# Optimization experiments

Measured on AMD Instinct MI355X. Metric: run time of the kernel, lower is better.

Reference implementation:

```python
import jax, jax.numpy as jnp
import numpy as np

G = 8192          # graphs per hand side (PyG batch)
J_SRC = 17        # source-hand joints (transform: Linear(17*64, 13*64))
J_TGT = 13        # target-hand joints
NEG_SLOPE = 0.01  # F.leaky_relu default


def _chain_edge_index(J, num_graphs):
    # bidirectional chain tree per graph, block-diagonal batched like PyG
    p = np.arange(J - 1); c = np.arange(1, J)
    src = np.concatenate([p, c]); dst = np.concatenate([c, p])
    base = np.arange(num_graphs)[:, None] * J
    return jnp.asarray(np.stack([(src[None] + base).ravel(), (dst[None] + base).ravel()]), jnp.int32)


def _lin_init(key, o, i):
    k1, k2 = jax.random.split(key)
    s = 1.0 / np.sqrt(i)
    return (jax.random.uniform(k1, (o, i), jnp.float32, -s, s),
            jax.random.uniform(k2, (o,), jnp.float32, -s, s))


def setup_inputs() -> dict:
    key = jax.random.key(0)
    ks = iter(jax.random.split(key, 64))
    inp = {}
    Nl = G * J_SRC
    inp["l_hand_x"] = jax.random.normal(next(ks), (Nl, 3), jnp.float32)
    inp["r_hand_x"] = jax.random.normal(next(ks), (Nl, 3), jnp.float32)
    ei_src = _chain_edge_index(J_SRC, G)
    inp["l_hand_edge_index"] = ei_src
    inp["r_hand_edge_index"] = ei_src
    E_src = ei_src.shape[1]
    inp["l_hand_edge_attr"] = jax.random.normal(next(ks), (E_src, 3), jnp.float32)
    inp["r_hand_edge_attr"] = jax.random.normal(next(ks), (E_src, 3), jnp.float32)
    ei_t = _chain_edge_index(J_TGT, G)
    inp["hand_edge_index"] = ei_t
    inp["hand_edge_attr"] = jax.random.normal(next(ks), (ei_t.shape[1], 6), jnp.float32)
    Nt = G * J_TGT
    inp["hand_lower"] = -(jax.random.uniform(next(ks), (Nt, 1), jnp.float32) + 0.5)
    inp["hand_upper"] = jax.random.uniform(next(ks), (Nt, 1), jnp.float32) + 0.5
    inp["hand_offset"] = jax.random.normal(next(ks), (Nt, 3), jnp.float32) * 0.05
    ax = jax.random.normal(next(ks), (Nt, 3), jnp.float32)
    inp["hand_axis"] = ax / jnp.linalg.norm(ax, axis=-1, keepdims=True)
    par = np.concatenate([[-1], np.arange(J_TGT - 1)])  # chain: root then parents
    inp["hand_parent"] = jnp.asarray(np.tile(par, G), jnp.int32)
    inp["num_graphs"] = G
    dims = {"enc1_lin": (16, 9),  "enc1_up": (16, 3),
            "enc2_lin": (32, 35), "enc2_up": (32, 16),
            "enc3_lin": (64, 67), "enc3_up": (64, 32),
            "trans":    (13 * 64, 17 * 64),
            "dec1_lin": (32, 138), "dec1_up": (32, 66),
            "dec2_lin": (16, 70),  "dec2_up": (16, 32),
            "dec3_lin": (1, 38),   "dec3_up": (1, 16)}
    for n, (o, i) in dims.items():
        W, b = _lin_init(next(ks), o, i)
        inp[n + "_W"] = W; inp[n + "_b"] = b
    return inp


def _block(x, ei, ea, Wl, bl, Wu, bu):
    # SpatialBasicBlock: gather x_i/x_j, concat edge_attr, linear+leaky_relu,
    # scatter-add at target nodes, residual upsample of x.
    src, dst = ei[0], ei[1]
    z = jnp.concatenate([x[dst], x[src], ea], axis=-1)  # [E, 2*in+edge]
    m = jax.nn.leaky_relu(z @ Wl.T + bl, NEG_SLOPE)
    agg = jax.ops.segment_sum(m, dst, num_segments=x.shape[0])
    return agg + x @ Wu.T + bu


def _rodrigues(ax, ang):
    # rotation matrices about unit axis ax [...,3] by angle ang [...]
    c = jnp.cos(ang)[..., None, None]; s = jnp.sin(ang)[..., None, None]
    I = jnp.eye(3, dtype=ax.dtype)
    aa = ax[..., :, None] * ax[..., None, :]
    x, y, z = ax[..., 0], ax[..., 1], ax[..., 2]
    zero = jnp.zeros_like(x)
    K = jnp.stack([jnp.stack([zero, -z, y], -1),
                   jnp.stack([z, zero, -x], -1),
                   jnp.stack([-y, x, zero], -1)], -2)
    return c * I + (1 - c) * aa + s * K


def _fk(ang, parent, offset, axis, num_graphs, J):
    # forward kinematics along parent chain (parent[j] < j, root = -1)
    a = ang.reshape(num_graphs, J)
    off = offset.reshape(num_graphs, J, 3)
    ax = axis.reshape(num_graphs, J, 3)
    par = parent.reshape(num_graphs, J)[0]  # same topology in every graph
    Rl = _rodrigues(ax, a)                  # [G, J, 3, 3] local rotations
    I = jnp.eye(3, dtype=ang.dtype)
    pos = jnp.zeros((num_graphs, J, 3), ang.dtype)
    rot = jnp.zeros((num_graphs, J, 3, 3), ang.dtype)
    for j in range(J):  # J=13 fixed structural loop
        p = par[j]
        root = p < 0
        Rp = jnp.where(root, I, jnp.take(rot, p, axis=1))
        Pp = jnp.where(root, 0.0, jnp.take(pos, p, axis=1))
        pos = pos.at[:, j].set(Pp + jnp.einsum('gab,gb->ga', Rp, off[:, j]))
        rot = rot.at[:, j].set(jnp.einsum('gab,gbc->gac', Rp, Rl[:, j]))
    return pos.reshape(-1, 3)


def reference(l_hand_x, r_hand_x, l_hand_edge_index, r_hand_edge_index,
              l_hand_edge_attr, r_hand_edge_attr, hand_edge_index, hand_edge_attr,
              hand_lower, hand_upper, hand_offset, hand_axis, hand_parent, num_graphs,
              enc1_lin_W, enc1_lin_b, enc1_up_W, enc1_up_b,
              enc2_lin_W, enc2_lin_b, enc2_up_W, enc2_up_b,
              enc3_lin_W, enc3_lin_b, enc3_up_W, enc3_up_b,
              trans_W, trans_b,
              dec1_lin_W, dec1_lin_b, dec1_up_W, dec1_up_b,
              dec2_lin_W, dec2_lin_b, dec2_up_W, dec2_up_b,
              dec3_lin_W, dec3_lin_b, dec3_up_W, dec3_up_b):
    # ---- encode ----
    Nl = l_hand_x.shape[0]
    x = jnp.concatenate([l_hand_x, r_hand_x], axis=0)
    ei = jnp.concatenate([l_hand_edge_index, r_hand_edge_index + Nl], axis=1)
    ea = jnp.concatenate([l_hand_edge_attr, r_hand_edge_attr], axis=0)
    h = _block(x, ei, ea, enc1_lin_W, enc1_lin_b, enc1_up_W, enc1_up_b)
    h = _block(h, ei, ea, enc2_lin_W, enc2_lin_b, enc2_up_W, enc2_up_b)
    h = _block(h, ei, ea, enc3_lin_W, enc3_lin_b, enc3_up_W, enc3_up_b)
    G2 = 2 * num_graphs
    z = jnp.tanh(h.reshape(G2, -1) @ trans_W.T + trans_b).reshape(-1, 64)
    # ---- decode ----
    half = z.shape[0] // 2
    ei_t = jnp.concatenate([hand_edge_index, hand_edge_index + half], axis=1)
    ea_t = jnp.concatenate([hand_edge_attr, hand_edge_attr], axis=0)
    lower = jnp.concatenate([hand_lower, hand_lower], axis=0)
    upper = jnp.concatenate([hand_upper, hand_upper], axis=0)
    offset = jnp.concatenate([hand_offset, hand_offset], axis=0)
    axis = jnp.concatenate([hand_axis, hand_axis], axis=0)
    parent = jnp.concatenate([hand_parent, hand_parent], axis=0)
    xd = jnp.concatenate([z, lower, upper], axis=1)  # [2*G*13, 66]
    h = _block(xd, ei_t, ea_t, dec1_lin_W, dec1_lin_b, dec1_up_W, dec1_up_b)
    h = _block(h, ei_t, ea_t, dec2_lin_W, dec2_lin_b, dec2_up_W, dec2_up_b)
    ang = jnp.tanh(_block(h, ei_t, ea_t, dec3_lin_W, dec3_lin_b, dec3_up_W, dec3_up_b))
    ang = lower + (upper - lower) * (ang + 1) / 2
    pos = _fk(ang, parent, offset, axis, G2, J_TGT)
    hn = ang.shape[0] // 2
    return ang[:hn], pos[:hn], ang[hn:], pos[hn:]
```

## Files before the change

kernel.cpp:

```cpp
#include <hip/hip_runtime.h>
#include <math.h>


constexpr int G_NUM = 8192;
constexpr int JS = 17;
constexpr int JT = 13;
constexpr int N_ENC = 2 * G_NUM * JS;
constexpr int N_DEC = 2 * G_NUM * JT;
constexpr int G2 = 2 * G_NUM;
constexpr int HN = G_NUM * JT;
constexpr int K_TR = JS * 64;
constexpr int N_TR = JT * 64;

typedef unsigned short u16;
typedef u16   u16x8 __attribute__((ext_vector_type(8)));
typedef u16   u16x4 __attribute__((ext_vector_type(4)));
typedef float f32x4 __attribute__((ext_vector_type(4)));
typedef __bf16 bf16x8 __attribute__((ext_vector_type(8)));

__device__ __forceinline__ float lrelu(float v) { return v > 0.f ? v : 0.01f * v; }
__device__ __forceinline__ u16 f2bf(float f) {
    unsigned u = __float_as_uint(f);
    u += 0x7fff + ((u >> 16) & 1);
    return (u16)(u >> 16);
}
__device__ __forceinline__ float bf2f(u16 h) { return __uint_as_float((unsigned)h << 16); }

template<int K_MM, int C_IN_W, int C_OUT, int C_E, int J, int G, bool TAIL>
__global__ __launch_bounds__(256)
void block_mfma(const u16* __restrict__ xHi, const u16* __restrict__ xLo,
                const float* __restrict__ eaA, const float* __restrict__ eaB, int g_half,
                const float* __restrict__ lowv, const float* __restrict__ upv,
                const float* __restrict__ Wl, const float* __restrict__ bl,
                const float* __restrict__ Wu, const float* __restrict__ bu,
                u16* __restrict__ outHi, u16* __restrict__ outLo)
{
    constexpr int ROWS = G * J;
    constexpr int F = (ROWS + 15) / 16;
    constexpr int NCH = C_OUT / 16;
    constexpr int KF = K_MM / 32;
    constexpr int KPAD = K_MM + 8;
    constexpr int EAS = 2 * (J - 1) * C_E;
    constexpr int CTOT = 2 * C_IN_W + C_E;
    constexpr int CW = (C_IN_W < K_MM) ? C_IN_W : K_MM;
    constexpr int WGG = 4 * G;

    __shared__ __align__(16) u16 sWH[3 * C_OUT * KPAD], sWL[3 * C_OUT * KPAD];
    __shared__ float sEA[WGG * EAS];
    __shared__ float sWe[C_OUT * C_E];
    __shared__ float sBl[C_OUT], sBu[C_OUT];
    __shared__ float sTl[TAIL ? 6 * C_OUT : 1];
    __shared__ float sLow[TAIL ? WGG * J : 1], sUpp[TAIL ? WGG * J : 1];

    const int t = threadIdx.x;
    const int g0 = blockIdx.x * WGG;

    for (int i = t; i < 3 * C_OUT * K_MM; i += 256) {
        const int ch = i / K_MM, k = i % K_MM;
        const int p = ch / C_OUT, o = ch % C_OUT;
        float v = 0.f;
        if (k < CW) {
            if (p == 0)      v = Wl[o * CTOT + k];
            else if (p == 1) v = Wl[o * CTOT + C_IN_W + k];
            else             v = Wu[o * C_IN_W + k];
        }
        const u16 h = f2bf(v);
        sWH[ch * KPAD + k] = h;
        sWL[ch * KPAD + k] = f2bf(v - bf2f(h));
    }
    for (int i = t; i < WGG * EAS; i += 256) {
        const int lg = i / EAS, r = i % EAS;
        const int g = g0 + lg;
        sEA[i] = (g < g_half) ? eaA[(size_t)g * EAS + r]
                              : eaB[(size_t)(g - g_half) * EAS + r];
    }
    for (int i = t; i < C_OUT * C_E; i += 256)
        sWe[i] = Wl[(i / C_E) * CTOT + 2 * C_IN_W + (i % C_E)];
    if (t < C_OUT) { sBl[t] = bl[t]; sBu[t] = bu[t]; }
    if constexpr (TAIL) {
        if (t < C_OUT) {
            sTl[t * 6 + 0] = Wl[t * CTOT + K_MM];
            sTl[t * 6 + 1] = Wl[t * CTOT + K_MM + 1];
            sTl[t * 6 + 2] = Wl[t * CTOT + C_IN_W + K_MM];
            sTl[t * 6 + 3] = Wl[t * CTOT + C_IN_W + K_MM + 1];
            sTl[t * 6 + 4] = Wu[t * C_IN_W + K_MM];
            sTl[t * 6 + 5] = Wu[t * C_IN_W + K_MM + 1];
        }
        for (int i = t; i < WGG * J; i += 256) {
            const int lg = i / J, j = i % J;
            const int g = g0 + lg;
            const int ge = (g < g_half) ? g : g - g_half;
            sLow[i] = lowv[ge * J + j];
            sUpp[i] = upv[ge * J + j];
        }
    }
    __syncthreads();

    const int wv = t >> 6, lane = t & 63;
    const int col = lane & 15, kg = lane >> 4;
    const size_t baseNode = (size_t)(blockIdx.x * 4 + wv) * ROWS;
    const int lgB = wv * G;

    for (int ch = 0; ch < NCH; ++ch) {
        const int o = ch * 16 + col;
        bf16x8 wUh[KF], wUl[KF], wVh[KF], wVl[KF], wPh[KF], wPl[KF];
        #pragma unroll
        for (int kf = 0; kf < KF; ++kf) {
            wUh[kf] = *(const bf16x8*)&sWH[(0 * C_OUT + o) * KPAD + kf * 32 + kg * 8];
            wUl[kf] = *(const bf16x8*)&sWL[(0 * C_OUT + o) * KPAD + kf * 32 + kg * 8];
            wVh[kf] = *(const bf16x8*)&sWH[(1 * C_OUT + o) * KPAD + kf * 32 + kg * 8];
            wVl[kf] = *(const bf16x8*)&sWL[(1 * C_OUT + o) * KPAD + kf * 32 + kg * 8];
            wPh[kf] = *(const bf16x8*)&sWH[(2 * C_OUT + o) * KPAD + kf * 32 + kg * 8];
            wPl[kf] = *(const bf16x8*)&sWL[(2 * C_OUT + o) * KPAD + kf * 32 + kg * 8];
        }
        float we[C_E];
        #pragma unroll
        for (int k = 0; k < C_E; ++k) we[k] = sWe[o * C_E + k];
        const float blo = sBl[o], buo = sBu[o];
        float tl0 = 0, tl1 = 0, tl2 = 0, tl3 = 0, tl4 = 0, tl5 = 0;
        if constexpr (TAIL) {
            tl0 = sTl[o * 6 + 0]; tl1 = sTl[o * 6 + 1]; tl2 = sTl[o * 6 + 2];
            tl3 = sTl[o * 6 + 3]; tl4 = sTl[o * 6 + 4]; tl5 = sTl[o * 6 + 5];
        }

        f32x4 Vpp = {0,0,0,0}, Vp = {0,0,0,0};
        f32x4 Up = {0,0,0,0}, Pp = {0,0,0,0};
        #pragma unroll
        for (int f = 0; f <= F; ++f) {
            f32x4 Vc = {0,0,0,0}, Uc = {0,0,0,0}, Pc = {0,0,0,0};
            if (f < F) {
                const int nrow = f * 16 + col;
                const size_t nd = baseNode + (nrow < ROWS ? nrow : ROWS - 1);
                #pragma unroll
                for (int kf = 0; kf < KF; ++kf) {
                    const bf16x8 aH = *(const bf16x8*)&xHi[nd * K_MM + kf * 32 + kg * 8];
                    const bf16x8 aL = *(const bf16x8*)&xLo[nd * K_MM + kf * 32 + kg * 8];
                    Vc = __builtin_amdgcn_mfma_f32_16x16x32_bf16(aH, wVh[kf], Vc, 0, 0, 0);
                    Vc = __builtin_amdgcn_mfma_f32_16x16x32_bf16(aH, wVl[kf], Vc, 0, 0, 0);
                    Vc = __builtin_amdgcn_mfma_f32_16x16x32_bf16(aL, wVh[kf], Vc, 0, 0, 0);
                    Uc = __builtin_amdgcn_mfma_f32_16x16x32_bf16(aH, wUh[kf], Uc, 0, 0, 0);
                    Uc = __builtin_amdgcn_mfma_f32_16x16x32_bf16(aH, wUl[kf], Uc, 0, 0, 0);
                    Uc = __builtin_amdgcn_mfma_f32_16x16x32_bf16(aL, wUh[kf], Uc, 0, 0, 0);
                    Pc = __builtin_amdgcn_mfma_f32_16x16x32_bf16(aH, wPh[kf], Pc, 0, 0, 0);
                    Pc = __builtin_amdgcn_mfma_f32_16x16x32_bf16(aH, wPl[kf], Pc, 0, 0, 0);
                    Pc = __builtin_amdgcn_mfma_f32_16x16x32_bf16(aL, wPh[kf], Pc, 0, 0, 0);
                }
            }
            if (f >= 1) {
                const int fm = f - 1;
                const float vL0a = __shfl(Vpp[3], 48 + col);
                const float vL0b = __shfl(Vp[3], (lane - 16) & 63);
                const float vL0 = (kg == 0) ? vL0a : vL0b;
                const float vR3a = __shfl(Vc[0], col);
                const float vR3b = __shfl(Vp[0], (lane + 16) & 63);
                const float vR3 = (kg == 3) ? vR3a : vR3b;
                #pragma unroll
                for (int r = 0; r < 4; ++r) {
                    const int row = fm * 16 + kg * 4 + r;
                    const bool valid = row < ROWS;
                    const int jpos = row % J;
                    int gl = row / J; if (gl > G - 1) gl = G - 1;
                    const int lg = lgB + gl;
                    const bool h1m = valid && (jpos > 0);
                    const bool h2m = valid && (jpos < J - 1);
                    const int jm = jpos > 0 ? jpos - 1 : 0;
                    float e1 = 0.f, e2 = 0.f;
                    #pragma unroll
                    for (int k = 0; k < C_E; ++k) {
                        e1 = fmaf(we[k], sEA[lg * EAS + jm * C_E + k], e1);
                        e2 = fmaf(we[k], sEA[lg * EAS + (J - 1 + jpos) * C_E + k], e2);
                    }
                    float vL = (r == 0) ? vL0 : Vp[r - 1];
                    float vR = (r == 3) ? vR3 : Vp[r + 1];
                    float u = Up[r], p = Pp[r];
                    if constexpr (TAIL) {
                        const int jp = jpos < J - 1 ? jpos + 1 : J - 1;
                        u = fmaf(tl0, sLow[lg * J + jpos], u);
                        u = fmaf(tl1, sUpp[lg * J + jpos], u);
                        p = fmaf(tl4, sLow[lg * J + jpos], p);
                        p = fmaf(tl5, sUpp[lg * J + jpos], p);
                        vL = fmaf(tl2, sLow[lg * J + jm], vL);
                        vL = fmaf(tl3, sUpp[lg * J + jm], vL);
                        vR = fmaf(tl2, sLow[lg * J + jp], vR);
                        vR = fmaf(tl3, sUpp[lg * J + jp], vR);
                    }
                    const float m1 = u + vL + e1 + blo;
                    const float m2 = u + vR + e2 + blo;
                    const float res = p + buo + (h1m ? lrelu(m1) : 0.f) + (h2m ? lrelu(m2) : 0.f);
                    if (valid) {
                        const size_t node = baseNode + row;
                        const u16 hh = f2bf(res);
                        outHi[node * C_OUT + o] = hh;
                        outLo[node * C_OUT + o] = f2bf(res - bf2f(hh));
                    }
                }
            }
            Vpp = Vp; Vp = Vc; Up = Uc; Pp = Pc;
        }
    }
}

template<int C_IN, int C_OUT, int C_E, int J, int NN, int OPAD>
__global__ __launch_bounds__(256)
void block_small(const float* __restrict__ xA, const float* __restrict__ xB, int node_half,
                 const float* __restrict__ eaA, const float* __restrict__ eaB, int g_half,
                 const float* __restrict__ Wl, const float* __restrict__ bl,
                 const float* __restrict__ Wu, const float* __restrict__ bu,
                 u16* __restrict__ outHi, u16* __restrict__ outLo, int N)
{
    constexpr int CTOT = 2 * C_IN + C_E;
    constexpr int SOP = C_OUT + 1;
    constexpr int NPB = 256 / C_OUT;
    __shared__ float wl_T[CTOT * SOP];
    __shared__ float wu_T[C_IN * SOP];
    __shared__ float bl_s[C_OUT], bu_s[C_OUT];
    const int t = threadIdx.x;
    for (int i = t; i < C_OUT * CTOT; i += 256) { int oo = i / CTOT, kk = i % CTOT; wl_T[kk * SOP + oo] = Wl[i]; }
    for (int i = t; i < C_OUT * C_IN; i += 256) { int oo = i / C_IN, kk = i % C_IN; wu_T[kk * SOP + oo] = Wu[i]; }
    if (t < C_OUT) { bl_s[t] = bl[t]; bu_s[t] = bu[t]; }
    __syncthreads();

    const int o = t % C_OUT;
    const int s = t / C_OUT;
    const int nb = (blockIdx.x * NPB + s) * NN;
    float up[NN], m1[NN], m2[NN];
    #pragma unroll
    for (int i = 0; i < NN; ++i) { up[i] = bu_s[o]; m1[i] = bl_s[o]; m2[i] = bl_s[o]; }
    auto clampn = [&](int nd) { return nd < 0 ? 0 : (nd >= N ? N - 1 : nd); };

    for (int k = 0; k < C_IN; ++k) {
        const float w0 = wl_T[k * SOP + o];
        const float w1 = wl_T[(C_IN + k) * SOP + o];
        const float wuv = wu_T[k * SOP + o];
        float xs[NN + 2];
        #pragma unroll
        for (int i = 0; i < NN + 2; ++i) {
            const int nd = clampn(nb - 1 + i);
            xs[i] = (nd < node_half) ? xA[(size_t)nd * C_IN + k]
                                     : xB[(size_t)(nd - node_half) * C_IN + k];
        }
        #pragma unroll
        for (int nd = 0; nd < NN; ++nd) {
            up[nd] = fmaf(wuv, xs[nd + 1], up[nd]);
            m1[nd] = fmaf(w0, xs[nd + 1], m1[nd]);
            m1[nd] = fmaf(w1, xs[nd], m1[nd]);
            m2[nd] = fmaf(w0, xs[nd + 1], m2[nd]);
            m2[nd] = fmaf(w1, xs[nd + 2], m2[nd]);
        }
    }
    #pragma unroll
    for (int nd = 0; nd < NN; ++nd) {
        const int node = nb + nd;
        const int g = node / J;
        const int j = node - g * J;
        const bool has1 = (j > 0), has2 = (j < J - 1);
        const int geff = (g < g_half) ? g : g - g_half;
        const float* ea = (g < g_half) ? eaA : eaB;
        const ptrdiff_t e1 = ((ptrdiff_t)geff * 2 * (J - 1) + (j - 1)) * C_E;
        const ptrdiff_t e2 = ((ptrdiff_t)geff * 2 * (J - 1) + (J - 1) + j) * C_E;
        float a1 = m1[nd], a2 = m2[nd];
        #pragma unroll
        for (int k = 0; k < C_E; ++k) {
            const float w = wl_T[(2 * C_IN + k) * SOP + o];
            if (has1) a1 = fmaf(w, ea[e1 + k], a1);
            if (has2) a2 = fmaf(w, ea[e2 + k], a2);
        }
        const float v = up[nd] + (has1 ? lrelu(a1) : 0.f) + (has2 ? lrelu(a2) : 0.f);
        const u16 hh = f2bf(v);
        outHi[(size_t)node * OPAD + o] = hh;
        outLo[(size_t)node * OPAD + o] = f2bf(v - bf2f(hh));
        if (OPAD > C_OUT) {
            outHi[(size_t)node * OPAD + o + C_OUT] = 0;
            outLo[(size_t)node * OPAD + o + C_OUT] = 0;
        }
    }
}

__device__ __forceinline__ void trans_step(const u16* __restrict__ sWHb,
                                           const u16* __restrict__ sWLb,
                                           const u16x8* __restrict__ a,
                                           int wn, int lr, int kg, f32x4 acc[4][2])
{
    bf16x8 bh[2], bl2[2];
    #pragma unroll
    for (int n = 0; n < 2; ++n) {
        const int r = wn * 32 + n * 16 + lr;
        bh[n]  = *(const bf16x8*)&sWHb[r * 40 + kg * 8];
        bl2[n] = *(const bf16x8*)&sWLb[r * 40 + kg * 8];
    }
    #pragma unroll
    for (int m = 0; m < 4; ++m) {
        const bf16x8 ah = __builtin_bit_cast(bf16x8, a[2 * m]);
        const bf16x8 al = __builtin_bit_cast(bf16x8, a[2 * m + 1]);
        #pragma unroll
        for (int n = 0; n < 2; ++n) {
            acc[m][n] = __builtin_amdgcn_mfma_f32_16x16x32_bf16(ah, bh[n],  acc[m][n], 0, 0, 0);
            acc[m][n] = __builtin_amdgcn_mfma_f32_16x16x32_bf16(ah, bl2[n], acc[m][n], 0, 0, 0);
            acc[m][n] = __builtin_amdgcn_mfma_f32_16x16x32_bf16(al, bh[n],  acc[m][n], 0, 0, 0);
        }
    }
}

__global__ __launch_bounds__(256)
void trans_mfma(const u16* __restrict__ aHi, const u16* __restrict__ aLo,
                const float* __restrict__ W, const float* __restrict__ bias,
                u16* __restrict__ zHi, u16* __restrict__ zLo)
{
    constexpr int NI = K_TR / 32;
    __shared__ __align__(16) u16 sWH[2][64 * 40], sWL[2][64 * 40];
    const int t = threadIdx.x, lane = t & 63, w = t >> 6;
    const int wm = w >> 1, wn = w & 1, lr = lane & 15, kg = lane >> 4;
    const int bm = blockIdx.x * 128, bn = blockIdx.y * 64;
    const int swr = t >> 2, swc = (t & 3) * 8;

    auto stageW = [&](int i, int buf) {
        const int k0 = i * 32;
        const float4 f0 = *(const float4*)&W[(size_t)(bn + swr) * K_TR + k0 + swc];
        const float4 f1 = *(const float4*)&W[(size_t)(bn + swr) * K_TR + k0 + swc + 4];
        const float fv[8] = {f0.x, f0.y, f0.z, f0.w, f1.x, f1.y, f1.z, f1.w};
        u16x8 hq, lq;
        #pragma unroll
        for (int j = 0; j < 8; ++j) {
            const u16 h = f2bf(fv[j]);
            hq[j] = h;
            lq[j] = f2bf(fv[j] - bf2f(h));
        }
        *(u16x8*)&sWH[buf][swr * 40 + swc] = hq;
        *(u16x8*)&sWL[buf][swr * 40 + swc] = lq;
    };
    u16x8 aA[8], aB[8];
    auto gloadA = [&](int i, u16x8* dst) {
        const int k0 = i * 32;
        #pragma unroll
        for (int m = 0; m < 4; ++m) {
            const size_t off = (size_t)(bm + wm * 64 + m * 16 + lr) * K_TR + k0 + kg * 8;
            dst[2 * m]     = *(const u16x8*)&aHi[off];
            dst[2 * m + 1] = *(const u16x8*)&aLo[off];
        }
    };

    f32x4 acc[4][2];
    #pragma unroll
    for (int m = 0; m < 4; ++m)
        #pragma unroll
        for (int n = 0; n < 2; ++n) acc[m][n] = f32x4{0.f, 0.f, 0.f, 0.f};

    stageW(0, 0);
    gloadA(0, aA);
    __syncthreads();
    for (int i = 0; i < NI; i += 2) {
        if (i + 1 < NI) { stageW(i + 1, 1); gloadA(i + 1, aB); }
        trans_step(sWH[0], sWL[0], aA, wn, lr, kg, acc);
        __syncthreads();
        if (i + 2 < NI) { stageW(i + 2, 0); gloadA(i + 2, aA); }
        trans_step(sWH[1], sWL[1], aB, wn, lr, kg, acc);
        __syncthreads();
    }

    #pragma unroll
    for (int n = 0; n < 2; ++n) {
        const int colz = bn + wn * 32 + n * 16 + lr;
        const float bv = bias[colz];
        #pragma unroll
        for (int m = 0; m < 4; ++m)
            #pragma unroll
            for (int r = 0; r < 4; ++r) {
                const int row = bm + wm * 64 + m * 16 + kg * 4 + r;
                const float v = tanhf(acc[m][n][r] + bv);
                const size_t idx = (size_t)row * N_TR + colz;
                const u16 hh = f2bf(v);
                zHi[idx] = hh;
                zLo[idx] = f2bf(v - bf2f(hh));
            }
    }
}

__global__ __launch_bounds__(256)
void dec3fk_kernel(const u16* __restrict__ xHi, const u16* __restrict__ xLo,
                   const float* __restrict__ ea,
                   const float* __restrict__ Wl, const float* __restrict__ bl,
                   const float* __restrict__ Wu, const float* __restrict__ bu,
                   const float* __restrict__ lowv, const float* __restrict__ upv,
                   const float* __restrict__ offset, const float* __restrict__ axis,
                   float* __restrict__ dout)
{
    const int g2 = blockIdx.x * 256 + threadIdx.x;
    if (g2 >= G2) return;
    const int geff = (g2 >= G_NUM) ? g2 - G_NUM : g2;
    const bool rightH = (g2 >= G_NUM);

    auto loadrow = [&](int nd, float* x) {
        const u16x8 h0 = *(const u16x8*)&xHi[(size_t)nd * 16];
        const u16x8 h1 = *(const u16x8*)&xHi[(size_t)nd * 16 + 8];
        const u16x8 l0 = *(const u16x8*)&xLo[(size_t)nd * 16];
        const u16x8 l1 = *(const u16x8*)&xLo[(size_t)nd * 16 + 8];
        #pragma unroll
        for (int k = 0; k < 8; ++k) {
            x[k]     = bf2f(h0[k]) + bf2f(l0[k]);
            x[k + 8] = bf2f(h1[k]) + bf2f(l1[k]);
        }
    };

    float xprev[16], xcur[16], xnext[16];
    #pragma unroll
    for (int k = 0; k < 16; ++k) xprev[k] = 0.f;
    loadrow(g2 * JT, xcur);
    loadrow(g2 * JT + 1, xnext);

    float R[9];
    float px = 0.f, py = 0.f, pz = 0.f;
    for (int j = 0; j < JT; ++j) {
        const int node = g2 * JT + j;
        const bool has1 = (j > 0), has2 = (j < JT - 1);
        float m1 = bl[0], m2 = m1, up = bu[0];
        #pragma unroll
        for (int k = 0; k < 16; ++k) {
            const float xd = xcur[k];
            up = fmaf(Wu[k], xd, up);
            const float w0 = Wl[k];
            m1 = fmaf(w0, xd, m1);
            m2 = fmaf(w0, xd, m2);
            const float w1 = Wl[16 + k];
            m1 = fmaf(w1, xprev[k], m1);
            m2 = fmaf(w1, xnext[k], m2);
        }
        const int e1 = (geff * 24 + (j - 1)) * 6;
        const int e2 = (geff * 24 + 12 + j) * 6;
        #pragma unroll
        for (int k = 0; k < 6; ++k) {
            const float ww = Wl[32 + k];
            if (has1) m1 = fmaf(ww, ea[e1 + k], m1);
            if (has2) m2 = fmaf(ww, ea[e2 + k], m2);
        }
        const float v = up + (has1 ? lrelu(m1) : 0.f) + (has2 ? lrelu(m2) : 0.f);
        const int idx = geff * JT + j;
        const float lo = lowv[idx], hi = upv[idx];
        const float a = lo + (hi - lo) * (tanhf(v) + 1.f) * 0.5f;
        if (!rightH) dout[node] = a;
        else         dout[4 * HN + idx] = a;

        const float ax = axis[idx * 3], ay = axis[idx * 3 + 1], az = axis[idx * 3 + 2];
        const float ox = offset[idx * 3], oy = offset[idx * 3 + 1], oz = offset[idx * 3 + 2];
        const float c = cosf(a), s = sinf(a), ic = 1.f - c;
        const float L[9] = {
            c + ic * ax * ax,      ic * ax * ay - s * az, ic * ax * az + s * ay,
            ic * ay * ax + s * az, c + ic * ay * ay,      ic * ay * az - s * ax,
            ic * az * ax - s * ay, ic * az * ay + s * ax, c + ic * az * az };
        if (j == 0) {
            px = ox; py = oy; pz = oz;
            #pragma unroll
            for (int q = 0; q < 9; ++q) R[q] = L[q];
        } else {
            px += R[0] * ox + R[1] * oy + R[2] * oz;
            py += R[3] * ox + R[4] * oy + R[5] * oz;
            pz += R[6] * ox + R[7] * oy + R[8] * oz;
            float T[9];
            #pragma unroll
            for (int r = 0; r < 3; ++r)
                #pragma unroll
                for (int cc = 0; cc < 3; ++cc)
                    T[r * 3 + cc] = R[r * 3] * L[cc] + R[r * 3 + 1] * L[3 + cc] + R[r * 3 + 2] * L[6 + cc];
            #pragma unroll
            for (int q = 0; q < 9; ++q) R[q] = T[q];
        }
        const int pbase = (!rightH) ? (HN + node * 3) : (5 * HN + idx * 3);
        dout[pbase] = px; dout[pbase + 1] = py; dout[pbase + 2] = pz;

        #pragma unroll
        for (int k = 0; k < 16; ++k) { xprev[k] = xcur[k]; xcur[k] = xnext[k]; }
        const int nn = node + 2 < N_DEC ? node + 2 : N_DEC - 1;
        if (j < JT - 1) loadrow(nn, xnext);
    }
}

extern "C" void kernel_launch(void* const* d_in, const int* in_sizes, int n_in,
                              void* d_out, int out_size, void* d_ws, size_t ws_size,
                              hipStream_t stream)
{
    const float* l_x  = (const float*)d_in[0];
    const float* r_x  = (const float*)d_in[1];
    const float* l_ea = (const float*)d_in[4];
    const float* r_ea = (const float*)d_in[5];
    const float* ea_t = (const float*)d_in[7];
    const float* lowv = (const float*)d_in[8];
    const float* upv  = (const float*)d_in[9];
    const float* offs = (const float*)d_in[10];
    const float* axis = (const float*)d_in[11];
    const float* e1lW = (const float*)d_in[14]; const float* e1lB = (const float*)d_in[15];
    const float* e1uW = (const float*)d_in[16]; const float* e1uB = (const float*)d_in[17];
    const float* e2lW = (const float*)d_in[18]; const float* e2lB = (const float*)d_in[19];
    const float* e2uW = (const float*)d_in[20]; const float* e2uB = (const float*)d_in[21];
    const float* e3lW = (const float*)d_in[22]; const float* e3lB = (const float*)d_in[23];
    const float* e3uW = (const float*)d_in[24]; const float* e3uB = (const float*)d_in[25];
    const float* trW  = (const float*)d_in[26]; const float* trB  = (const float*)d_in[27];
    const float* d1lW = (const float*)d_in[28]; const float* d1lB = (const float*)d_in[29];
    const float* d1uW = (const float*)d_in[30]; const float* d1uB = (const float*)d_in[31];
    const float* d2lW = (const float*)d_in[32]; const float* d2lB = (const float*)d_in[33];
    const float* d2uW = (const float*)d_in[34]; const float* d2uB = (const float*)d_in[35];
    const float* d3lW = (const float*)d_in[36]; const float* d3lB = (const float*)d_in[37];
    const float* d3uW = (const float*)d_in[38]; const float* d3uB = (const float*)d_in[39];

    char* ws = (char*)d_ws;
    u16* h1H  = (u16*)(ws + 0);          u16* h1L  = (u16*)(ws + 17825792);
    u16* h2H  = (u16*)(ws + 71303168);   u16* h2L  = (u16*)(ws + 89128960);
    u16* aH   = (u16*)(ws + 0);          u16* aL   = (u16*)(ws + 35651584);
    u16* zzH  = (u16*)(ws + 71303168);   u16* zzL  = (u16*)(ws + 98566144);
    u16* hd1H = (u16*)(ws + 0);          u16* hd1L = (u16*)(ws + 13631488);
    u16* hd2H = (u16*)(ws + 27262976);   u16* hd2L = (u16*)(ws + 34078720);
    float* outp = (float*)d_out;

    block_small<3, 16, 3, JS, 4, 32><<<N_ENC / 64, 256, 0, stream>>>(
        l_x, r_x, G_NUM * JS, l_ea, r_ea, G_NUM,
        e1lW, e1lB, e1uW, e1uB, h1H, h1L, N_ENC);
    block_mfma<32, 16, 32, 3, JS, 4, false><<<1024, 256, 0, stream>>>(
        h1H, h1L, l_ea, r_ea, G_NUM, nullptr, nullptr,
        e2lW, e2lB, e2uW, e2uB, h2H, h2L);
    block_mfma<32, 32, 64, 3, JS, 4, false><<<1024, 256, 0, stream>>>(
        h2H, h2L, l_ea, r_ea, G_NUM, nullptr, nullptr,
        e3lW, e3lB, e3uW, e3uB, aH, aL);
    trans_mfma<<<dim3(G2 / 128, N_TR / 64), 256, 0, stream>>>(aH, aL, trW, trB, zzH, zzL);
    block_mfma<64, 66, 32, 6, JT, 4, true><<<1024, 256, 0, stream>>>(
        zzH, zzL, ea_t, ea_t, G_NUM, lowv, upv,
        d1lW, d1lB, d1uW, d1uB, hd1H, hd1L);
    block_mfma<32, 32, 16, 6, JT, 4, false><<<1024, 256, 0, stream>>>(
        hd1H, hd1L, ea_t, ea_t, G_NUM, nullptr, nullptr,
        d2lW, d2lB, d2uW, d2uB, hd2H, hd2L);
    dec3fk_kernel<<<(G2 + 255) / 256, 256, 0, stream>>>(
        hd2H, hd2L, ea_t, d3lW, d3lB, d3uW, d3uB, lowv, upv, offs, axis, outp);
}
```

Before: 633.8 us.

## Enlarge trans GEMM tile to 128x128 and stage A operand through LDS

Result: faster. 527.0 us (-16.8%).

```diff
diff --git a/kernel.cpp b/kernel.cpp
--- a/kernel.cpp
+++ b/kernel.cpp
@@ -276,102 +276,112 @@
     }
 }
 
-__device__ __forceinline__ void trans_step(const u16* __restrict__ sWHb,
-                                           const u16* __restrict__ sWLb,
-                                           const u16x8* __restrict__ a,
-                                           int wn, int lr, int kg, f32x4 acc[4][2])
-{
-    bf16x8 bh[2], bl2[2];
-    #pragma unroll
-    for (int n = 0; n < 2; ++n) {
-        const int r = wn * 32 + n * 16 + lr;
-        bh[n]  = *(const bf16x8*)&sWHb[r * 40 + kg * 8];
-        bl2[n] = *(const bf16x8*)&sWLb[r * 40 + kg * 8];
-    }
-    #pragma unroll
-    for (int m = 0; m < 4; ++m) {
-        const bf16x8 ah = __builtin_bit_cast(bf16x8, a[2 * m]);
-        const bf16x8 al = __builtin_bit_cast(bf16x8, a[2 * m + 1]);
-        #pragma unroll
-        for (int n = 0; n < 2; ++n) {
-            acc[m][n] = __builtin_amdgcn_mfma_f32_16x16x32_bf16(ah, bh[n],  acc[m][n], 0, 0, 0);
-            acc[m][n] = __builtin_amdgcn_mfma_f32_16x16x32_bf16(ah, bl2[n], acc[m][n], 0, 0, 0);
-            acc[m][n] = __builtin_amdgcn_mfma_f32_16x16x32_bf16(al, bh[n],  acc[m][n], 0, 0, 0);
-        }
-    }
-}
-
 __global__ __launch_bounds__(256)
 void trans_mfma(const u16* __restrict__ aHi, const u16* __restrict__ aLo,
                 const float* __restrict__ W, const float* __restrict__ bias,
                 u16* __restrict__ zHi, u16* __restrict__ zLo)
 {
     constexpr int NI = K_TR / 32;
-    __shared__ __align__(16) u16 sWH[2][64 * 40], sWL[2][64 * 40];
+    constexpr int ST = 40;
+    __shared__ __align__(16) u16 sAH[2][128 * ST], sAL[2][128 * ST];
+    __shared__ __align__(16) u16 sBH[2][128 * ST], sBL[2][128 * ST];
     const int t = threadIdx.x, lane = t & 63, w = t >> 6;
     const int wm = w >> 1, wn = w & 1, lr = lane & 15, kg = lane >> 4;
-    const int bm = blockIdx.x * 128, bn = blockIdx.y * 64;
-    const int swr = t >> 2, swc = (t & 3) * 8;
-
-    auto stageW = [&](int i, int buf) {
+    const int bm = blockIdx.x * 128, bn = blockIdx.y * 128;
+    const int sr = t >> 1, sc = (t & 1) * 16;
+
+    u16x8 rA[4];
+    float4 rW[4];
+    auto gload = [&](int i) {
         const int k0 = i * 32;
-        const float4 f0 = *(const float4*)&W[(size_t)(bn + swr) * K_TR + k0 + swc];
-        const float4 f1 = *(const float4*)&W[(size_t)(bn + swr) * K_TR + k0 + swc + 4];
-        const float fv[8] = {f0.x, f0.y, f0.z, f0.w, f1.x, f1.y, f1.z, f1.w};
-        u16x8 hq, lq;
-        #pragma unroll
-        for (int j = 0; j < 8; ++j) {
-            const u16 h = f2bf(fv[j]);
-            hq[j] = h;
-            lq[j] = f2bf(fv[j] - bf2f(h));
-        }
-        *(u16x8*)&sWH[buf][swr * 40 + swc] = hq;
-        *(u16x8*)&sWL[buf][swr * 40 + swc] = lq;
+        const size_t oa = (size_t)(bm + sr) * K_TR + k0 + sc;
+        rA[0] = *(const u16x8*)&aHi[oa];
+        rA[1] = *(const u16x8*)&aHi[oa + 8];
+        rA[2] = *(const u16x8*)&aLo[oa];
+        rA[3] = *(const u16x8*)&aLo[oa + 8];
+        int wrow = bn + sr; if (wrow > N_TR - 1) wrow = N_TR - 1;
+        const size_t ow = (size_t)wrow * K_TR + k0 + sc;
+        rW[0] = *(const float4*)&W[ow];
+        rW[1] = *(const float4*)&W[ow + 4];
+        rW[2] = *(const float4*)&W[ow + 8];
+        rW[3] = *(const float4*)&W[ow + 12];
     };
-    u16x8 aA[8], aB[8];
-    auto gloadA = [&](int i, u16x8* dst) {
-        const int k0 = i * 32;
-        #pragma unroll
-        for (int m = 0; m < 4; ++m) {
-            const size_t off = (size_t)(bm + wm * 64 + m * 16 + lr) * K_TR + k0 + kg * 8;
-            dst[2 * m]     = *(const u16x8*)&aHi[off];
-            dst[2 * m + 1] = *(const u16x8*)&aLo[off];
-        }
+    auto stage = [&](int buf) {
+        *(u16x8*)&sAH[buf][sr * ST + sc]     = rA[0];
+        *(u16x8*)&sAH[buf][sr * ST + sc + 8] = rA[1];
+        *(u16x8*)&sAL[buf][sr * ST + sc]     = rA[2];
+        *(u16x8*)&sAL[buf][sr * ST + sc + 8] = rA[3];
+        u16x8 hq0{}, lq0{}, hq1{}, lq1{};
+        auto sp0 = [&](float f, int j) { const u16 h = f2bf(f); hq0[j] = h; lq0[j] = f2bf(f - bf2f(h)); };
+        auto sp1 = [&](float f, int j) { const u16 h = f2bf(f); hq1[j] = h; lq1[j] = f2bf(f - bf2f(h)); };
+        sp0(rW[0].x, 0); sp0(rW[0].y, 1); sp0(rW[0].z, 2); sp0(rW[0].w, 3);
+        sp0(rW[1].x, 4); sp0(rW[1].y, 5); sp0(rW[1].z, 6); sp0(rW[1].w, 7);
+        sp1(rW[2].x, 0); sp1(rW[2].y, 1); sp1(rW[2].z, 2); sp1(rW[2].w, 3);
+        sp1(rW[3].x, 4); sp1(rW[3].y, 5); sp1(rW[3].z, 6); sp1(rW[3].w, 7);
+        *(u16x8*)&sBH[buf][sr * ST + sc]     = hq0;
+        *(u16x8*)&sBH[buf][sr * ST + sc + 8] = hq1;
+        *(u16x8*)&sBL[buf][sr * ST + sc]     = lq0;
+        *(u16x8*)&sBL[buf][sr * ST + sc + 8] = lq1;
     };
 
-    f32x4 acc[4][2];
+    f32x4 acc[4][4];
     #pragma unroll
     for (int m = 0; m < 4; ++m)
         #pragma unroll
-        for (int n = 0; n < 2; ++n) acc[m][n] = f32x4{0.f, 0.f, 0.f, 0.f};
-
-    stageW(0, 0);
-    gloadA(0, aA);
-    __syncthreads();
-    for (int i = 0; i < NI; i += 2) {
-        if (i + 1 < NI) { stageW(i + 1, 1); gloadA(i + 1, aB); }
-        trans_step(sWH[0], sWL[0], aA, wn, lr, kg, acc);
-        __syncthreads();
-        if (i + 2 < NI) { stageW(i + 2, 0); gloadA(i + 2, aA); }
-        trans_step(sWH[1], sWL[1], aB, wn, lr, kg, acc);
-        __syncthreads();
-    }
-
-    #pragma unroll
-    for (int n = 0; n < 2; ++n) {
-        const int colz = bn + wn * 32 + n * 16 + lr;
-        const float bv = bias[colz];
+        for (int n = 0; n < 4; ++n) acc[m][n] = f32x4{0.f, 0.f, 0.f, 0.f};
+
+    auto step = [&](int buf) {
+        bf16x8 ah[4], al[4], bh[4], bl2[4];
+        #pragma unroll
+        for (int m = 0; m < 4; ++m) {
+            const int r = wm * 64 + m * 16 + lr;
+            ah[m] = *(const bf16x8*)&sAH[buf][r * ST + kg * 8];
+            al[m] = *(const bf16x8*)&sAL[buf][r * ST + kg * 8];
+        }
+        #pragma unroll
+        for (int n = 0; n < 4; ++n) {
+            const int r = wn * 64 + n * 16 + lr;
+            bh[n]  = *(const bf16x8*)&sBH[buf][r * ST + kg * 8];
+            bl2[n] = *(const bf16x8*)&sBL[buf][r * ST + kg * 8];
+        }
         #pragma unroll
         for (int m = 0; m < 4; ++m)
             #pragma unroll
-            for (int r = 0; r < 4; ++r) {
-                const int row = bm + wm * 64 + m * 16 + kg * 4 + r;
-                const float v = tanhf(acc[m][n][r] + bv);
-                const size_t idx = (size_t)row * N_TR + colz;
-                const u16 hh = f2bf(v);
-                zHi[idx] = hh;
-                zLo[idx] = f2bf(v - bf2f(hh));
+            for (int n = 0; n < 4; ++n) {
+                acc[m][n] = __builtin_amdgcn_mfma_f32_16x16x32_bf16(ah[m], bh[n],  acc[m][n], 0, 0, 0);
+                acc[m][n] = __builtin_amdgcn_mfma_f32_16x16x32_bf16(ah[m], bl2[n], acc[m][n], 0, 0, 0);
+                acc[m][n] = __builtin_amdgcn_mfma_f32_16x16x32_bf16(al[m], bh[n],  acc[m][n], 0, 0, 0);
             }
+    };
+
+    gload(0);
+    stage(0);
+    __syncthreads();
+    for (int i = 0; i < NI; ++i) {
+        const int buf = i & 1;
+        if (i + 1 < NI) gload(i + 1);
+        step(buf);
+        if (i + 1 < NI) stage(buf ^ 1);
+        __syncthreads();
+    }
+
+    #pragma unroll
+    for (int n = 0; n < 4; ++n) {
+        const int colz = bn + wn * 64 + n * 16 + lr;
+        if (colz < N_TR) {
+            const float bv = bias[colz];
+            #pragma unroll
+            for (int m = 0; m < 4; ++m)
+                #pragma unroll
+                for (int r = 0; r < 4; ++r) {
+                    const int row = bm + wm * 64 + m * 16 + kg * 4 + r;
+                    const float v = tanhf(acc[m][n][r] + bv);
+                    const size_t idx = (size_t)row * N_TR + colz;
+                    const u16 hh = f2bf(v);
+                    zHi[idx] = hh;
+                    zLo[idx] = f2bf(v - bf2f(hh));
+                }
+        }
     }
 }
 
@@ -518,7 +528,8 @@
     block_mfma<32, 32, 64, 3, JS, 4, false><<<1024, 256, 0, stream>>>(
         h2H, h2L, l_ea, r_ea, G_NUM, nullptr, nullptr,
         e3lW, e3lB, e3uW, e3uB, aH, aL);
-    trans_mfma<<<dim3(G2 / 128, N_TR / 64), 256, 0, stream>>>(aH, aL, trW, trB, zzH, zzL);
+    trans_mfma<<<dim3(G2 / 128, (N_TR + 127) / 128), 256, 0, stream>>>(
+        aH, aL, trW, trB, zzH, zzL);
     block_mfma<64, 66, 32, 6, JT, 4, true><<<1024, 256, 0, stream>>>(
         zzH, zzL, ea_t, ea_t, G_NUM, lowv, upv,
         d1lW, d1lB, d1uW, d1uB, hd1H, hd1L);
```
